# Optimization experiments

Measured on AMD Instinct MI355X. Metric: run time of the kernel, lower is better.

The kernel has to match this reference:

```python
import jax, jax.numpy as jnp
import numpy as np

NUM_HEADS = 16
DIM = 1024
N_TOKENS = 2048
S0 = 8            # number of frames
P = N_TOKENS // S0  # tokens per frame
B = 1


def setup_inputs() -> dict:
    key = jax.random.key(0)
    ks = jax.random.split(key, 8)
    C = DIM
    x = jax.random.normal(ks[0], (B, N_TOKENS, C), dtype=jnp.float32)
    # nn.Linear-style weights (out_features, in_features), scaled ~1/sqrt(fan_in)
    Wqkv = jax.random.normal(ks[1], (3 * C, C), dtype=jnp.float32) * (C ** -0.5)
    bqkv = jnp.zeros((3 * C,), dtype=jnp.float32)
    Wproj = jax.random.normal(ks[2], (C, C), dtype=jnp.float32) * (C ** -0.5)
    bproj = jnp.zeros((C,), dtype=jnp.float32)
    frame_bias = jax.random.normal(ks[3], (S0, S0), dtype=jnp.float32) * 0.5
    # frame adjacency: random sparsity pattern, diagonal always allowed
    adj = jax.random.bernoulli(ks[4], 0.25, (S0, S0))
    adj = adj | jnp.eye(S0, dtype=bool)
    frame_ids = (jnp.arange(N_TOKENS) // P).astype(jnp.int64)
    is_hub = jax.random.bernoulli(ks[5], 0.05, (N_TOKENS,))
    return {
        'x': x, 'Wqkv': Wqkv, 'bqkv': bqkv, 'Wproj': Wproj, 'bproj': bproj,
        'frame_bias': frame_bias, 'adj': adj, 'frame_ids': frame_ids,
        'is_hub': is_hub,
    }


def _sparse_attention(x, Wqkv, bqkv, Wproj, bproj, frame_bias, adj, frame_ids, is_hub):
    Bx, N, C = x.shape
    H = NUM_HEADS
    D = C // H
    scale = D ** -0.5
    # qkv projection -> q,k,v each [B,H,N,D]
    qkv = x @ Wqkv.T + bqkv                      # [B,N,3C]
    qkv = qkv.reshape(Bx, N, 3, H, D).transpose(2, 0, 3, 1, 4)
    q, k, v = qkv[0], qkv[1], qkv[2]

    # token-level mask derived from frame-level structures (score_mod semantics)
    fi = frame_ids                               # [N]
    adj_allowed = adj[fi[:, None], fi[None, :]]  # [N,N] bool
    same_frame = fi[:, None] == fi[None, :]
    neither_hub = ~(is_hub[:, None] | is_hub[None, :])
    hub_allowed = same_frame | neither_hub       # mask_hub_tokens=True
    allowed = adj_allowed & hub_allowed
    bias = frame_bias[fi[:, None], fi[None, :]]  # soft_mask=True

    scores = jnp.einsum('bhqd,bhkd->bhqk', q, k) * scale
    scores = jnp.where(allowed, scores + bias, -jnp.inf)
    attn = jax.nn.softmax(scores, axis=-1)
    out = jnp.einsum('bhqk,bhkd->bhqd', attn, v)
    out = out.transpose(0, 2, 1, 3).reshape(Bx, N, C)
    return out @ Wproj.T + bproj


def reference(x, Wqkv, bqkv, Wproj, bproj, frame_bias, adj, frame_ids, is_hub):
    return _sparse_attention(x, Wqkv, bqkv, Wproj, bproj, frame_bias,
                             adj, frame_ids, is_hub)
```

## Files before the change

### kernel.cpp

```cpp
#include <hip/hip_runtime.h>
#include <hip/hip_bf16.h>
#include <math.h>

#define NTOK 2048
#define CDIM 1024
#define NHEAD 16
#define HDIM 64

typedef __attribute__((ext_vector_type(8))) short bf16x8;
typedef __attribute__((ext_vector_type(4))) float f32x4;
typedef __attribute__((ext_vector_type(4))) unsigned int u32x4;

__device__ inline unsigned short bf16_rn(float f) {
    unsigned int u = __float_as_uint(f);
    u += 0x7FFFu + ((u >> 16) & 1u);
    return (unsigned short)(u >> 16);
}

template <int N> __device__ inline void waitcnt_vm() {
    if constexpr (N == 0) asm volatile("s_waitcnt vmcnt(0)" ::: "memory");
    else if constexpr (N == 4) asm volatile("s_waitcnt vmcnt(4)" ::: "memory");
    else if constexpr (N == 6) asm volatile("s_waitcnt vmcnt(6)" ::: "memory");
}

__device__ inline void gload16(const void* g, void* l) {
    __builtin_amdgcn_global_load_lds((const __attribute__((address_space(1))) void*)g,
                                     (__attribute__((address_space(3))) void*)l,
                                     16, 0, 0);
}

__global__ __launch_bounds__(256) void conv3(const float* __restrict__ s0, unsigned short* __restrict__ h0, int nb0,
                                             const float* __restrict__ s1, unsigned short* __restrict__ h1, int nb1,
                                             const float* __restrict__ s2, unsigned short* __restrict__ h2) {
    int b = blockIdx.x;
    const float* s;
    unsigned short* hh;
    if (b < nb0) { s = s0; hh = h0; }
    else if (b < nb0 + nb1) { s = s1; hh = h1; b -= nb0; }
    else { s = s2; hh = h2; b -= nb0 + nb1; }
    const int i = b * 256 + threadIdx.x;
    float4 v = ((const float4*)s)[i];
    ushort4 h;
    h.x = bf16_rn(v.x); h.y = bf16_rn(v.y); h.z = bf16_rn(v.z); h.w = bf16_rn(v.w);
    ((ushort4*)hh)[i] = h;
}

template <int BM, int BN, int M, int N, int K, int MODE>
__global__ __launch_bounds__(256) void gemm_mfma(const unsigned short* __restrict__ Ah,
                                                 const unsigned short* __restrict__ Bh,
                                                 const float* __restrict__ bias,
                                                 float* __restrict__ C,
                                                 unsigned short* __restrict__ qfb,
                                                 unsigned short* __restrict__ kfb,
                                                 unsigned short* __restrict__ vfb) {
    constexpr int BK = 64;
    constexpr int FM = BM / 32;
    constexpr int FN = BN / 32;
    constexpr int ASZ = BM * BK;
    constexpr int BSZ = BN * BK;
    constexpr int BUF = ASZ + BSZ;
    __shared__ unsigned short lds[2 * BUF];

    const int tid = threadIdx.x;
    const int lane = tid & 63;
    const int w = tid >> 6;
    const int m0 = blockIdx.y * BM;
    const int n0 = blockIdx.x * BN;
    const int wave_m = (w >> 1) * (BM / 2);
    const int wave_n = (w & 1) * (BN / 2);
    const int lr = lane & 15;
    const int kg_ = lane >> 4;
    const int srow = tid >> 3;
    const int scol = (tid & 7) * 8;

    const size_t aRow = (size_t)(m0 + srow) * K + scol;
    const size_t bRow = (size_t)(n0 + srow) * K + scol;

    f32x4 acc[FM][FN];
#pragma unroll
    for (int i = 0; i < FM; ++i)
#pragma unroll
        for (int j = 0; j < FN; ++j) acc[i][j] = {0.f, 0.f, 0.f, 0.f};

    auto stage = [&](int buf, int k0) {
        unsigned short* bb = lds + buf * BUF;
#pragma unroll
        for (int j = 0; j < BM / 32; ++j)
            gload16(Ah + aRow + (size_t)j * 32 * K + k0, bb + (srow + j * 32) * BK + scol);
#pragma unroll
        for (int j = 0; j < BN / 32; ++j)
            gload16(Bh + bRow + (size_t)j * 32 * K + k0, bb + ASZ + (srow + j * 32) * BK + scol);
    };

    stage(0, 0);
    constexpr int NL = BM / 32 + BN / 32;
    constexpr int NT = K / BK;
    for (int t = 0; t < NT; ++t) {
        const int cur = t & 1;
        if (t + 1 < NT) {
            stage(cur ^ 1, (t + 1) * BK);
            waitcnt_vm<NL>();
        } else {
            waitcnt_vm<0>();
        }
        __builtin_amdgcn_s_barrier();

        const unsigned short* bb = lds + cur * BUF;
        bf16x8 ah[FM][2], bh[FN][2];
#pragma unroll
        for (int f = 0; f < FM; ++f)
#pragma unroll
            for (int ks = 0; ks < 2; ++ks)
                ah[f][ks] = *(const bf16x8*)&bb[(wave_m + f * 16 + lr) * BK + ks * 32 + kg_ * 8];
#pragma unroll
        for (int f = 0; f < FN; ++f)
#pragma unroll
            for (int ks = 0; ks < 2; ++ks)
                bh[f][ks] = *(const bf16x8*)&bb[ASZ + (wave_n + f * 16 + lr) * BK + ks * 32 + kg_ * 8];
        __builtin_amdgcn_s_setprio(1);
#pragma unroll
        for (int ks = 0; ks < 2; ++ks)
#pragma unroll
            for (int fm = 0; fm < FM; ++fm)
#pragma unroll
                for (int fn = 0; fn < FN; ++fn)
                    acc[fm][fn] = __builtin_amdgcn_mfma_f32_16x16x32_bf16(ah[fm][ks], bh[fn][ks], acc[fm][fn], 0, 0, 0);
        __builtin_amdgcn_s_setprio(0);
        asm volatile("" ::: "memory");
        __builtin_amdgcn_s_barrier();
    }

    if constexpr (MODE == 2) {
        float bv[FN];
#pragma unroll
        for (int fn = 0; fn < FN; ++fn) bv[fn] = bias[n0 + wave_n + fn * 16 + lr];
#pragma unroll
        for (int fm = 0; fm < FM; ++fm) {
            const int row0 = m0 + wave_m + fm * 16 + kg_ * 4;
#pragma unroll
            for (int fn = 0; fn < FN; ++fn) {
                const int col = n0 + wave_n + fn * 16 + lr;
#pragma unroll
                for (int r = 0; r < 4; ++r)
                    C[(size_t)(row0 + r) * N + col] = acc[fm][fn][r] + bv[fn];
            }
        }
    } else {
        const int reg = n0 >> 10;
        if (reg == 2) {
#pragma unroll
            for (int fn = 0; fn < FN; ++fn) {
                const int col = n0 + wave_n + fn * 16 + lr;
                const int head = (col >> 6) & 15;
                const int d = col & 63;
                const float bv = bias[col];
#pragma unroll
                for (int fm = 0; fm < FM; ++fm) {
                    const int tok = m0 + wave_m + fm * 16 + kg_ * 4;
                    const int tile = tok >> 6;
                    const int t6 = tok & 63;
                    const int c = t6 >> 5;
                    const int t5 = t6 & 31;
                    const int hi = (t5 >> 4) & 1;
                    const int kgv = (t5 >> 2) & 3;
                    const int fd = d >> 4;
                    const int lrv = d & 15;
                    ushort4 pk;
                    pk.x = bf16_rn(acc[fm][fn][0] + bv);
                    pk.y = bf16_rn(acc[fm][fn][1] + bv);
                    pk.z = bf16_rn(acc[fm][fn][2] + bv);
                    pk.w = bf16_rn(acc[fm][fn][3] + bv);
                    const size_t idx = (((size_t)((head * 32 + tile) * 2 + c) * 4 + fd) * 64 +
                                        (kgv * 16 + lrv)) * 8 + hi * 4;
                    *(ushort4*)&vfb[idx] = pk;
                }
            }
        } else {
            float* sOut = (float*)lds;
            float bv[FN];
#pragma unroll
            for (int fn = 0; fn < FN; ++fn) bv[fn] = bias[n0 + wave_n + fn * 16 + lr];
#pragma unroll
            for (int fm = 0; fm < FM; ++fm) {
                const int row0 = wave_m + fm * 16 + kg_ * 4;
#pragma unroll
                for (int fn = 0; fn < FN; ++fn) {
                    const int col = wave_n + fn * 16 + lr;
#pragma unroll
                    for (int r = 0; r < 4; ++r)
                        sOut[(row0 + r) * 132 + col] = acc[fm][fn][r] + bv[fn];
                }
            }
            __syncthreads();
            const float sc = (reg == 0) ? 0.125f : 1.0f;
            unsigned short* dp = (reg == 0) ? qfb : kfb;
            const int tokL = tid >> 2;
            const int tokG = m0 + tokL;
            const int lrk = tokG & 15;
#pragma unroll
            for (int j = 0; j < 4; ++j) {
                const int ch = (tid & 3) + j * 4;
                const int dcol = ch * 8;
                const int gcol = n0 + dcol;
                const int head = (gcol >> 6) & 15;
                const int d = gcol & 63;
                const int dc = d >> 5;
                const int kgq = (d >> 3) & 3;
                float4 v0 = *(float4*)&sOut[tokL * 132 + dcol];
                float4 v1 = *(float4*)&sOut[tokL * 132 + dcol + 4];
                bf16x8 pk;
                pk[0] = (short)bf16_rn(v0.x * sc);
                pk[1] = (short)bf16_rn(v0.y * sc);
                pk[2] = (short)bf16_rn(v0.z * sc);
                pk[3] = (short)bf16_rn(v0.w * sc);
                pk[4] = (short)bf16_rn(v1.x * sc);
                pk[5] = (short)bf16_rn(v1.y * sc);
                pk[6] = (short)bf16_rn(v1.z * sc);
                pk[7] = (short)bf16_rn(v1.w * sc);
                size_t idx;
                if (reg == 1)
                    idx = (((size_t)((head * 32 + (tokG >> 6)) * 4 + ((tokG >> 4) & 3)) * 2 + dc) * 64 +
                           (kgq * 16 + lrk)) * 8;
                else
                    idx = (((size_t)(head * 128 + (tokG >> 4)) * 2 + dc) * 64 +
                           (kgq * 16 + lrk)) * 8;
                *(bf16x8*)&dp[idx] = pk;
            }
        }
    }
}

__global__ __launch_bounds__(128, 4) void attn_mfma(const unsigned short* __restrict__ qfb,
                                                    const unsigned short* __restrict__ kfb,
                                                    const unsigned short* __restrict__ vfb,
                                                    const float* __restrict__ frame_bias,
                                                    const int* __restrict__ adj,
                                                    const int* __restrict__ is_hub,
                                                    unsigned short* __restrict__ ath) {
    __shared__ float sM[64][18];
    __shared__ int sList[32];
    __shared__ float sFB[8];
    __shared__ unsigned long long sHub[32];
    __shared__ int sNT;

    const int bid = blockIdx.x;
    const int r8 = bid & 7, tt = bid >> 3;
    const int q16 = tt & 127, hb = tt >> 7;
    const int h = r8 * 2 + hb;
    const int q0 = q16 * 16;

    const int tid = threadIdx.x;
    const int lane = tid & 63;
    const int w = tid >> 6;
    const int lr = lane & 15;
    const int kg = lane >> 4;
    const int fi = q0 >> 8;

    const unsigned short* qb = qfb + ((size_t)(h * 128 + q16) * 2) * 512;
    bf16x8 qh[2];
    qh[0] = *(const bf16x8*)&qb[lane * 8];
    qh[1] = *(const bf16x8*)&qb[512 + lane * 8];
    const bool hq = is_hub[q0 + lr] != 0;

#pragma unroll
    for (int i = 0; i < 16; ++i) {
        const int t2 = w * 16 + i;
        unsigned long long mb = __ballot(is_hub[t2 * 64 + lane] != 0);
        if (lane == 0) sHub[t2] = mb;
    }
    if (tid < 8) sFB[tid] = frame_bias[fi * 8 + tid];
    if (w == 0) {
        const bool ok = (lane < 32) && (adj[fi * 8 + ((lane & 31) >> 2)] != 0);
        const unsigned long long am = __ballot(ok);
        if (lane == 0) {
            int c = 0;
#pragma unroll 1
            for (int t2 = 0; t2 < 32; ++t2)
                if ((am >> t2) & 1ull) sList[c++] = t2;
            sNT = c;
        }
    }
    __syncthreads();
    const int nt = sNT;

    const unsigned short* kb = kfb + (size_t)(h * 32) * 4096;
    const unsigned short* vb = vfb + (size_t)(h * 32) * 4096;

    float m_i = -INFINITY, l_i = 0.f;
    f32x4 oacc[4];
#pragma unroll
    for (int fd = 0; fd < 4; ++fd) oacc[fd] = {0.f, 0.f, 0.f, 0.f};

#pragma unroll 1
    for (int i = w; i < nt; i += 2) {
        const int tile = sList[i];
        const size_t tbase = (size_t)tile * 4096 + lane * 8;
        const int fj = tile >> 2;
        const bool same = (fj == fi);
        const float biasv = sFB[fj];
        const unsigned long long hubmask = sHub[tile];

        bf16x8 kfr[4][2];
#pragma unroll
        for (int fk = 0; fk < 4; ++fk)
#pragma unroll
            for (int dc = 0; dc < 2; ++dc)
                kfr[fk][dc] = *(const bf16x8*)&kb[tbase + (fk * 2 + dc) * 512];

        f32x4 sacc[4];
#pragma unroll
        for (int fk = 0; fk < 4; ++fk) sacc[fk] = {0.f, 0.f, 0.f, 0.f};
        __builtin_amdgcn_s_setprio(1);
#pragma unroll
        for (int fk = 0; fk < 4; ++fk)
#pragma unroll
            for (int dc = 0; dc < 2; ++dc)
                sacc[fk] = __builtin_amdgcn_mfma_f32_16x16x32_bf16(kfr[fk][dc], qh[dc], sacc[fk], 0, 0, 0);
        __builtin_amdgcn_s_setprio(0);

        bf16x8 vfr[2][4];
#pragma unroll
        for (int c = 0; c < 2; ++c)
#pragma unroll
            for (int fd = 0; fd < 4; ++fd)
                vfr[c][fd] = *(const bf16x8*)&vb[tbase + (c * 4 + fd) * 512];

        float sv[4][4];
        float rmax = -INFINITY;
#pragma unroll
        for (int fk = 0; fk < 4; ++fk)
#pragma unroll
            for (int r = 0; r < 4; ++r) {
                float val = sacc[fk][r] + biasv;
                if (!same) {
                    const int k = fk * 16 + kg * 4 + r;
                    if (hq || ((hubmask >> k) & 1ull)) val = -INFINITY;
                }
                sv[fk][r] = val;
                rmax = fmaxf(rmax, val);
            }
        rmax = fmaxf(rmax, __shfl_xor(rmax, 16));
        rmax = fmaxf(rmax, __shfl_xor(rmax, 32));

        if (!__all(rmax <= m_i + 8.f)) {
            const float mn = fmaxf(m_i, rmax);
            const float alpha = (m_i == -INFINITY) ? 0.f : __expf(m_i - mn);
            m_i = mn;
            l_i *= alpha;
#pragma unroll
            for (int fd = 0; fd < 4; ++fd) {
                oacc[fd][0] *= alpha; oacc[fd][1] *= alpha;
                oacc[fd][2] *= alpha; oacc[fd][3] *= alpha;
            }
        }

        float p4[4][4];
        float psum = 0.f;
#pragma unroll
        for (int fk = 0; fk < 4; ++fk)
#pragma unroll
            for (int r = 0; r < 4; ++r) {
                const float pv = (sv[fk][r] == -INFINITY) ? 0.f : __expf(sv[fk][r] - m_i);
                p4[fk][r] = pv;
                psum += pv;
            }
        psum += __shfl_xor(psum, 16);
        psum += __shfl_xor(psum, 32);
        l_i += psum;

        unsigned int pc[4][2];
#pragma unroll
        for (int fk = 0; fk < 4; ++fk)
#pragma unroll
            for (int rp = 0; rp < 2; ++rp)
                pc[fk][rp] = (unsigned int)bf16_rn(p4[fk][2 * rp]) |
                             ((unsigned int)bf16_rn(p4[fk][2 * rp + 1]) << 16);
        __builtin_amdgcn_s_setprio(1);
#pragma unroll
        for (int c = 0; c < 2; ++c) {
            u32x4 pw = {pc[2 * c][0], pc[2 * c][1], pc[2 * c + 1][0], pc[2 * c + 1][1]};
            bf16x8 pbv = __builtin_bit_cast(bf16x8, pw);
#pragma unroll
            for (int fd = 0; fd < 4; ++fd)
                oacc[fd] = __builtin_amdgcn_mfma_f32_16x16x32_bf16(vfr[c][fd], pbv, oacc[fd], 0, 0, 0);
        }
        __builtin_amdgcn_s_setprio(0);
    }

    if (w == 1) {
        float* mp = &sM[lane][0];
        mp[0] = m_i;
        mp[1] = l_i;
#pragma unroll
        for (int fd = 0; fd < 4; ++fd)
#pragma unroll
            for (int r = 0; r < 4; ++r) mp[2 + fd * 4 + r] = oacc[fd][r];
    }
    __syncthreads();
    if (w == 0) {
        const float mb = sM[lane][0];
        const float lb = sM[lane][1];
        const float m = fmaxf(m_i, mb);
        const float aa = (m_i == -INFINITY) ? 0.f : __expf(m_i - m);
        const float ab = (mb == -INFINITY) ? 0.f : __expf(mb - m);
        const float inv = 1.f / (l_i * aa + lb * ab);
#pragma unroll
        for (int fd = 0; fd < 4; ++fd) {
            ushort4 h4;
            unsigned short hs[4];
#pragma unroll
            for (int r = 0; r < 4; ++r) {
                const float o = (oacc[fd][r] * aa + sM[lane][2 + fd * 4 + r] * ab) * inv;
                hs[r] = bf16_rn(o);
            }
            h4.x = hs[0]; h4.y = hs[1]; h4.z = hs[2]; h4.w = hs[3];
            const size_t idx = (size_t)(q0 + lr) * CDIM + h * 64 + fd * 16 + kg * 4;
            *(ushort4*)&ath[idx] = h4;
        }
    }
}

extern "C" void kernel_launch(void* const* d_in, const int* in_sizes, int n_in,
                              void* d_out, int out_size, void* d_ws, size_t ws_size,
                              hipStream_t stream) {
    const float* x          = (const float*)d_in[0];
    const float* Wqkv       = (const float*)d_in[1];
    const float* bqkv       = (const float*)d_in[2];
    const float* Wproj      = (const float*)d_in[3];
    const float* bproj      = (const float*)d_in[4];
    const float* frame_bias = (const float*)d_in[5];
    const int*   adj        = (const int*)d_in[6];
    const int*   is_hub     = (const int*)d_in[8];
    float* out = (float*)d_out;

    char* ws = (char*)d_ws;
    size_t off = 0;
    auto alloc_us = [&](size_t n) { unsigned short* p = (unsigned short*)(ws + off); off += n * 2; return p; };
    unsigned short* qfb = alloc_us((size_t)NHEAD * NTOK * HDIM);
    unsigned short* kfb = alloc_us((size_t)NHEAD * NTOK * HDIM);
    unsigned short* vfb = alloc_us((size_t)NHEAD * HDIM * NTOK);
    unsigned short* xh  = alloc_us((size_t)NTOK * CDIM);
    unsigned short* wqh = alloc_us((size_t)3 * CDIM * CDIM);
    unsigned short* wph = alloc_us((size_t)CDIM * CDIM);
    unsigned short* ath = alloc_us((size_t)NTOK * CDIM);

    const int nb_x = (NTOK * CDIM / 4) / 256;
    const int nb_wq = (3 * CDIM * CDIM / 4) / 256;
    const int nb_wp = (CDIM * CDIM / 4) / 256;
    conv3<<<nb_x + nb_wq + nb_wp, 256, 0, stream>>>(x, xh, nb_x,
                                                    Wqkv, wqh, nb_wq,
                                                    Wproj, wph);

    gemm_mfma<64, 128, NTOK, 3 * CDIM, CDIM, 1>
        <<<dim3((3 * CDIM) / 128, NTOK / 64), 256, 0, stream>>>(
            xh, wqh, bqkv, nullptr, qfb, kfb, vfb);
    attn_mfma<<<2048, 128, 0, stream>>>(qfb, kfb, vfb,
                                        frame_bias, adj, is_hub, ath);
    gemm_mfma<64, 64, NTOK, CDIM, CDIM, 2>
        <<<dim3(CDIM / 64, NTOK / 64), 256, 0, stream>>>(
            ath, wph, bproj, out, nullptr, nullptr, nullptr);
}
```

Before: 69.62 us.

## Process two 16-query groups per attention block to reuse K/V fragments

Each attention block now handles 32 queries (two 16-row groups) instead of 16, so every K and V fragment loaded from global memory feeds twice as many MFMAs. This halves the grid to 1024 blocks and loosens launch bounds to allow more registers for the doubled accumulators and softmax state. The aim is to cut redundant K/V global loads per query. In exchange there are fewer blocks to fill the GPU and higher register pressure, which lowers occupancy.

```diff
diff --git a/kernel.cpp b/kernel.cpp
--- a/kernel.cpp
+++ b/kernel.cpp
@@ -230,14 +230,14 @@
     }
 }
 
-__global__ __launch_bounds__(128, 4) void attn_mfma(const unsigned short* __restrict__ qfb,
+__global__ __launch_bounds__(128, 2) void attn_mfma(const unsigned short* __restrict__ qfb,
                                                     const unsigned short* __restrict__ kfb,
                                                     const unsigned short* __restrict__ vfb,
                                                     const float* __restrict__ frame_bias,
                                                     const int* __restrict__ adj,
                                                     const int* __restrict__ is_hub,
                                                     unsigned short* __restrict__ ath) {
-    __shared__ float sM[64][18];
+    __shared__ float sM[2][64][18];
     __shared__ int sList[32];
     __shared__ float sFB[8];
     __shared__ unsigned long long sHub[32];
@@ -245,9 +245,9 @@
 
     const int bid = blockIdx.x;
     const int r8 = bid & 7, tt = bid >> 3;
-    const int q16 = tt & 127, hb = tt >> 7;
+    const int q32 = tt & 63, hb = tt >> 6;
     const int h = r8 * 2 + hb;
-    const int q0 = q16 * 16;
+    const int q0 = q32 * 32;
 
     const int tid = threadIdx.x;
     const int lane = tid & 63;
@@ -256,11 +256,14 @@
     const int kg = lane >> 4;
     const int fi = q0 >> 8;
 
-    const unsigned short* qb = qfb + ((size_t)(h * 128 + q16) * 2) * 512;
-    bf16x8 qh[2];
-    qh[0] = *(const bf16x8*)&qb[lane * 8];
-    qh[1] = *(const bf16x8*)&qb[512 + lane * 8];
-    const bool hq = is_hub[q0 + lr] != 0;
+    const unsigned short* qbA = qfb + ((size_t)(h * 128 + 2 * q32) * 2) * 512;
+    bf16x8 qhA[2], qhB[2];
+    qhA[0] = *(const bf16x8*)&qbA[lane * 8];
+    qhA[1] = *(const bf16x8*)&qbA[512 + lane * 8];
+    qhB[0] = *(const bf16x8*)&qbA[1024 + lane * 8];
+    qhB[1] = *(const bf16x8*)&qbA[1536 + lane * 8];
+    const bool hqA = is_hub[q0 + lr] != 0;
+    const bool hqB = is_hub[q0 + 16 + lr] != 0;
 
 #pragma unroll
     for (int i = 0; i < 16; ++i) {
@@ -286,10 +289,10 @@
     const unsigned short* kb = kfb + (size_t)(h * 32) * 4096;
     const unsigned short* vb = vfb + (size_t)(h * 32) * 4096;
 
-    float m_i = -INFINITY, l_i = 0.f;
-    f32x4 oacc[4];
-#pragma unroll
-    for (int fd = 0; fd < 4; ++fd) oacc[fd] = {0.f, 0.f, 0.f, 0.f};
+    float mA = -INFINITY, lA = 0.f, mB = -INFINITY, lB = 0.f;
+    f32x4 oA[4], oB[4];
+#pragma unroll
+    for (int fd = 0; fd < 4; ++fd) { oA[fd] = {0.f, 0.f, 0.f, 0.f}; oB[fd] = {0.f, 0.f, 0.f, 0.f}; }
 
 #pragma unroll 1
     for (int i = w; i < nt; i += 2) {
@@ -307,15 +310,17 @@
             for (int dc = 0; dc < 2; ++dc)
                 kfr[fk][dc] = *(const bf16x8*)&kb[tbase + (fk * 2 + dc) * 512];
 
-        f32x4 sacc[4];
-#pragma unroll
-        for (int fk = 0; fk < 4; ++fk) sacc[fk] = {0.f, 0.f, 0.f, 0.f};
+        f32x4 sA[4], sB[4];
+#pragma unroll
+        for (int fk = 0; fk < 4; ++fk) { sA[fk] = {0.f, 0.f, 0.f, 0.f}; sB[fk] = {0.f, 0.f, 0.f, 0.f}; }
         __builtin_amdgcn_s_setprio(1);
 #pragma unroll
         for (int fk = 0; fk < 4; ++fk)
 #pragma unroll
-            for (int dc = 0; dc < 2; ++dc)
-                sacc[fk] = __builtin_amdgcn_mfma_f32_16x16x32_bf16(kfr[fk][dc], qh[dc], sacc[fk], 0, 0, 0);
+            for (int dc = 0; dc < 2; ++dc) {
+                sA[fk] = __builtin_amdgcn_mfma_f32_16x16x32_bf16(kfr[fk][dc], qhA[dc], sA[fk], 0, 0, 0);
+                sB[fk] = __builtin_amdgcn_mfma_f32_16x16x32_bf16(kfr[fk][dc], qhB[dc], sB[fk], 0, 0, 0);
+            }
         __builtin_amdgcn_s_setprio(0);
 
         bf16x8 vfr[2][4];
@@ -325,97 +330,115 @@
             for (int fd = 0; fd < 4; ++fd)
                 vfr[c][fd] = *(const bf16x8*)&vb[tbase + (c * 4 + fd) * 512];
 
-        float sv[4][4];
-        float rmax = -INFINITY;
-#pragma unroll
-        for (int fk = 0; fk < 4; ++fk)
-#pragma unroll
-            for (int r = 0; r < 4; ++r) {
-                float val = sacc[fk][r] + biasv;
-                if (!same) {
-                    const int k = fk * 16 + kg * 4 + r;
-                    if (hq || ((hubmask >> k) & 1ull)) val = -INFINITY;
-                }
-                sv[fk][r] = val;
-                rmax = fmaxf(rmax, val);
-            }
-        rmax = fmaxf(rmax, __shfl_xor(rmax, 16));
-        rmax = fmaxf(rmax, __shfl_xor(rmax, 32));
-
-        if (!__all(rmax <= m_i + 8.f)) {
-            const float mn = fmaxf(m_i, rmax);
-            const float alpha = (m_i == -INFINITY) ? 0.f : __expf(m_i - mn);
-            m_i = mn;
-            l_i *= alpha;
-#pragma unroll
-            for (int fd = 0; fd < 4; ++fd) {
-                oacc[fd][0] *= alpha; oacc[fd][1] *= alpha;
-                oacc[fd][2] *= alpha; oacc[fd][3] *= alpha;
-            }
-        }
-
-        float p4[4][4];
-        float psum = 0.f;
-#pragma unroll
-        for (int fk = 0; fk < 4; ++fk)
-#pragma unroll
-            for (int r = 0; r < 4; ++r) {
-                const float pv = (sv[fk][r] == -INFINITY) ? 0.f : __expf(sv[fk][r] - m_i);
-                p4[fk][r] = pv;
-                psum += pv;
-            }
-        psum += __shfl_xor(psum, 16);
-        psum += __shfl_xor(psum, 32);
-        l_i += psum;
-
-        unsigned int pc[4][2];
-#pragma unroll
-        for (int fk = 0; fk < 4; ++fk)
-#pragma unroll
-            for (int rp = 0; rp < 2; ++rp)
-                pc[fk][rp] = (unsigned int)bf16_rn(p4[fk][2 * rp]) |
-                             ((unsigned int)bf16_rn(p4[fk][2 * rp + 1]) << 16);
-        __builtin_amdgcn_s_setprio(1);
-#pragma unroll
-        for (int c = 0; c < 2; ++c) {
-            u32x4 pw = {pc[2 * c][0], pc[2 * c][1], pc[2 * c + 1][0], pc[2 * c + 1][1]};
-            bf16x8 pbv = __builtin_bit_cast(bf16x8, pw);
+#pragma unroll
+        for (int g = 0; g < 2; ++g) {
+            f32x4* sg = g ? sB : sA;
+            const bool hq = g ? hqB : hqA;
+            float& m_i = g ? mB : mA;
+            float& l_i = g ? lB : lA;
+            f32x4* oacc = g ? oB : oA;
+
+            float sv[4][4];
+            float rmax = -INFINITY;
+#pragma unroll
+            for (int fk = 0; fk < 4; ++fk)
+#pragma unroll
+                for (int r = 0; r < 4; ++r) {
+                    float val = sg[fk][r] + biasv;
+                    if (!same) {
+                        const int k = fk * 16 + kg * 4 + r;
+                        if (hq || ((hubmask >> k) & 1ull)) val = -INFINITY;
+                    }
+                    sv[fk][r] = val;
+                    rmax = fmaxf(rmax, val);
+                }
+            rmax = fmaxf(rmax, __shfl_xor(rmax, 16));
+            rmax = fmaxf(rmax, __shfl_xor(rmax, 32));
+
+            if (!__all(rmax <= m_i + 8.f)) {
+                const float mn = fmaxf(m_i, rmax);
+                const float alpha = (m_i == -INFINITY) ? 0.f : __expf(m_i - mn);
+                m_i = mn;
+                l_i *= alpha;
+#pragma unroll
+                for (int fd = 0; fd < 4; ++fd) {
+                    oacc[fd][0] *= alpha; oacc[fd][1] *= alpha;
+                    oacc[fd][2] *= alpha; oacc[fd][3] *= alpha;
+                }
+            }
+
+            float psum = 0.f;
+#pragma unroll
+            for (int fk = 0; fk < 4; ++fk)
+#pragma unroll
+                for (int r = 0; r < 4; ++r) {
+                    const float pv = (sv[fk][r] == -INFINITY) ? 0.f : __expf(sv[fk][r] - m_i);
+                    sv[fk][r] = pv;
+                    psum += pv;
+                }
+            psum += __shfl_xor(psum, 16);
+            psum += __shfl_xor(psum, 32);
+            l_i += psum;
+
+            unsigned int pc[4][2];
+#pragma unroll
+            for (int fk = 0; fk < 4; ++fk)
+#pragma unroll
+                for (int rp = 0; rp < 2; ++rp)
+                    pc[fk][rp] = (unsigned int)bf16_rn(sv[fk][2 * rp]) |
+                                 ((unsigned int)bf16_rn(sv[fk][2 * rp + 1]) << 16);
+            __builtin_amdgcn_s_setprio(1);
+#pragma unroll
+            for (int c = 0; c < 2; ++c) {
+                u32x4 pw = {pc[2 * c][0], pc[2 * c][1], pc[2 * c + 1][0], pc[2 * c + 1][1]};
+                bf16x8 pbv = __builtin_bit_cast(bf16x8, pw);
+#pragma unroll
+                for (int fd = 0; fd < 4; ++fd)
+                    oacc[fd] = __builtin_amdgcn_mfma_f32_16x16x32_bf16(vfr[c][fd], pbv, oacc[fd], 0, 0, 0);
+            }
+            __builtin_amdgcn_s_setprio(0);
+        }
+    }
+
+    if (w == 1) {
+#pragma unroll
+        for (int g = 0; g < 2; ++g) {
+            float* mp = &sM[g][lane][0];
+            mp[0] = g ? mB : mA;
+            mp[1] = g ? lB : lA;
+            const f32x4* oacc = g ? oB : oA;
 #pragma unroll
             for (int fd = 0; fd < 4; ++fd)
-                oacc[fd] = __builtin_amdgcn_mfma_f32_16x16x32_bf16(vfr[c][fd], pbv, oacc[fd], 0, 0, 0);
-        }
-        __builtin_amdgcn_s_setprio(0);
-    }
-
-    if (w == 1) {
-        float* mp = &sM[lane][0];
-        mp[0] = m_i;
-        mp[1] = l_i;
-#pragma unroll
-        for (int fd = 0; fd < 4; ++fd)
-#pragma unroll
-            for (int r = 0; r < 4; ++r) mp[2 + fd * 4 + r] = oacc[fd][r];
+#pragma unroll
+                for (int r = 0; r < 4; ++r) mp[2 + fd * 4 + r] = oacc[fd][r];
+        }
     }
     __syncthreads();
     if (w == 0) {
-        const float mb = sM[lane][0];
-        const float lb = sM[lane][1];
-        const float m = fmaxf(m_i, mb);
-        const float aa = (m_i == -INFINITY) ? 0.f : __expf(m_i - m);
-        const float ab = (mb == -INFINITY) ? 0.f : __expf(mb - m);
-        const float inv = 1.f / (l_i * aa + lb * ab);
-#pragma unroll
-        for (int fd = 0; fd < 4; ++fd) {
-            ushort4 h4;
-            unsigned short hs[4];
-#pragma unroll
-            for (int r = 0; r < 4; ++r) {
-                const float o = (oacc[fd][r] * aa + sM[lane][2 + fd * 4 + r] * ab) * inv;
-                hs[r] = bf16_rn(o);
-            }
-            h4.x = hs[0]; h4.y = hs[1]; h4.z = hs[2]; h4.w = hs[3];
-            const size_t idx = (size_t)(q0 + lr) * CDIM + h * 64 + fd * 16 + kg * 4;
-            *(ushort4*)&ath[idx] = h4;
+#pragma unroll
+        for (int g = 0; g < 2; ++g) {
+            const float m_i = g ? mB : mA;
+            const float l_i = g ? lB : lA;
+            const f32x4* oacc = g ? oB : oA;
+            const float mb = sM[g][lane][0];
+            const float lb = sM[g][lane][1];
+            const float m = fmaxf(m_i, mb);
+            const float aa = (m_i == -INFINITY) ? 0.f : __expf(m_i - m);
+            const float ab = (mb == -INFINITY) ? 0.f : __expf(mb - m);
+            const float inv = 1.f / (l_i * aa + lb * ab);
+#pragma unroll
+            for (int fd = 0; fd < 4; ++fd) {
+                ushort4 h4;
+                unsigned short hs[4];
+#pragma unroll
+                for (int r = 0; r < 4; ++r) {
+                    const float o = (oacc[fd][r] * aa + sM[g][lane][2 + fd * 4 + r] * ab) * inv;
+                    hs[r] = bf16_rn(o);
+                }
+                h4.x = hs[0]; h4.y = hs[1]; h4.z = hs[2]; h4.w = hs[3];
+                const size_t idx = (size_t)(q0 + g * 16 + lr) * CDIM + h * 64 + fd * 16 + kg * 4;
+                *(ushort4*)&ath[idx] = h4;
+            }
         }
     }
 }
@@ -454,7 +477,7 @@
     gemm_mfma<64, 128, NTOK, 3 * CDIM, CDIM, 1>
         <<<dim3((3 * CDIM) / 128, NTOK / 64), 256, 0, stream>>>(
             xh, wqh, bqkv, nullptr, qfb, kfb, vfb);
-    attn_mfma<<<2048, 128, 0, stream>>>(qfb, kfb, vfb,
+    attn_mfma<<<1024, 128, 0, stream>>>(qfb, kfb, vfb,
                                         frame_bias, adj, is_hub, ath);
     gemm_mfma<64, 64, NTOK, CDIM, CDIM, 2>
         <<<dim3(CDIM / 64, NTOK / 64), 256, 0, stream>>>(
```

Result: slower. 72.68 us (+4.4%).
